# Optimization experiments

Hardware: AMD Instinct MI355X
Metric: run time of the kernel (lower is better)

Reference implementation:

```python
import jax, jax.numpy as jnp
import numpy as np

HIDDEN = 300
ATOM_FDIM = 133
BOND_ONLY_FDIM = 14
BOND_FDIM = ATOM_FDIM + BOND_ONLY_FDIM  # 147, chemprop concatenates atom feats into bond feats
DEPTH = 3
N_ATOMS = 100000
N_BONDS = 200000  # directed bonds, stored as reverse pairs (2k, 2k+1)
MAX_NB = 6
N_MOLS = 2000


def _lin(key, fan_in, fan_out):
    s = 1.0 / np.sqrt(fan_in)
    return jax.random.uniform(key, (fan_in, fan_out), jnp.float32, -s, s)


def setup_inputs() -> dict:
    key = jax.random.key(0)
    ks = jax.random.split(key, 16)
    f_atoms = jax.random.normal(ks[0], (N_ATOMS, ATOM_FDIM), jnp.float32)
    f_bonds = jax.random.normal(ks[1], (N_BONDS, BOND_FDIM), jnp.float32)
    a2b = jax.random.randint(ks[2], (N_ATOMS, MAX_NB), 0, N_BONDS, jnp.int32)
    b2a = jax.random.randint(ks[3], (N_BONDS,), 0, N_ATOMS, jnp.int32)
    b2revb = jnp.arange(N_BONDS, dtype=jnp.int32) ^ 1  # reverse-bond pairing
    graph_idx = jnp.sort(jax.random.randint(ks[4], (N_ATOMS,), 0, N_MOLS, jnp.int32))
    params = dict(
        W_i=_lin(ks[5], BOND_FDIM, HIDDEN),              # no bias in chemprop W_i
        W_h=_lin(ks[6], HIDDEN, HIDDEN),                 # no bias in chemprop W_h
        W_o=_lin(ks[7], ATOM_FDIM + HIDDEN, HIDDEN),
        b_o=jnp.zeros((HIDDEN,), jnp.float32),
        W_node=_lin(ks[8], HIDDEN, ATOM_FDIM),
        b_node=jnp.zeros((ATOM_FDIM,), jnp.float32),
        W_edge=_lin(ks[9], HIDDEN, BOND_ONLY_FDIM),
        b_edge=jnp.zeros((BOND_ONLY_FDIM,), jnp.float32),
        W_g1=_lin(ks[10], HIDDEN, HIDDEN),
        b_g1=jnp.zeros((HIDDEN,), jnp.float32),
        W_g2=_lin(ks[11], HIDDEN, 1),
        b_g2=jnp.zeros((1,), jnp.float32),
    )
    return dict(f_atoms=f_atoms, f_bonds=f_bonds, a2b=a2b, b2a=b2a,
                b2revb=b2revb, graph_idx=graph_idx, **params)


def reference(f_atoms, f_bonds, a2b, b2a, b2revb, graph_idx,
              W_i, W_h, W_o, b_o, W_node, b_node,
              W_edge, b_edge, W_g1, b_g1, W_g2, b_g2):
    # ---- chemprop bond-message MPN encoder (dropout=0) ----
    inp = f_bonds @ W_i                       # [n_bonds, H]
    msg = jax.nn.relu(inp)
    for _ in range(DEPTH - 1):
        a_msg = msg[a2b].sum(axis=1)          # gather neighbor bond msgs -> [n_atoms, H]
        msg = jax.nn.relu(inp + (a_msg[b2a] - msg[b2revb]) @ W_h)
    a_msg = msg[a2b].sum(axis=1)
    atom_hiddens = jax.nn.relu(jnp.concatenate([f_atoms, a_msg], axis=-1) @ W_o + b_o)
    # ---- graph pooling: per-molecule SUM (as in the forward loop) ----
    graph_emb = jax.ops.segment_sum(atom_hiddens, graph_idx, num_segments=N_MOLS)
    # ---- heads ----
    node_preds = atom_hiddens @ W_node + b_node
    # bond loop: visits each reverse pair once (even bond first), averages endpoint atoms
    e1 = jnp.arange(0, N_BONDS, 2)
    a1 = b2a[e1]
    a2 = b2a[b2revb[e1]]
    h_avg = 0.5 * (atom_hiddens[a1] + atom_hiddens[a2])
    edge_preds = h_avg @ W_edge + b_edge
    graph_preds = jax.nn.relu(graph_emb @ W_g1 + b_g1) @ W_g2 + b_g2
    return node_preds, edge_preds, graph_preds
```

## Files before the change

### kernel.cpp

```cpp
#include <hip/hip_runtime.h>

typedef unsigned short u16;
typedef unsigned int u32;

#define N_ATOMS 100000
#define N_BONDS 200000
#define N_EDGES 100000
#define HIDDEN 300
#define HP 320
#define ATOM_FDIM 133
#define BOND_FDIM 147
#define CATP 448
#define N_MOLS 2000

typedef __bf16 bf16x8 __attribute__((ext_vector_type(8)));
typedef float f32x4 __attribute__((ext_vector_type(4)));

__device__ __forceinline__ u16 f2bf(float f) {
    union { float f; u32 u; } x; x.f = f;
    u32 u = x.u;
    u32 r = u + 0x7fffu + ((u >> 16) & 1u);
    return (u16)(r >> 16);
}
__device__ __forceinline__ float bf2f(u16 h) {
    union { u32 u; float f; } x; x.u = ((u32)h) << 16;
    return x.f;
}

union U8 { uint4 v; u16 h[8]; };
union U4 { uint2 v; u16 h[4]; };

template<int ASRC, int EP, int KSTEPS, int NB>
__global__ __launch_bounds__(256) void k_gemmR(
    const u16* __restrict__ srcA, const float* __restrict__ fsrc,
    int M, const u16* __restrict__ Bt, int ldb, int Nout,
    const float* __restrict__ bias, const float* __restrict__ bias2,
    u16* __restrict__ O1, float* __restrict__ F1, float* __restrict__ F2,
    const u16* __restrict__ inp_in, int nwg)
{
    __shared__ __align__(16) u16 As[128 * 40];
    __shared__ __align__(16) u16 Bs[64 * 40];

    const int bid = blockIdx.x;
    const int q = nwg >> 3, r = nwg & 7;
    const int xcd = bid & 7, sidx = bid >> 3;
    const int wg = (xcd < r ? xcd * (q + 1) : r * (q + 1) + (xcd - r) * q) + sidx;

    const int n0 = (wg % NB) * 64;
    const int row0 = (wg / NB) * 128;

    const int tid = threadIdx.x;
    const int lane = tid & 63;
    const int w = tid >> 6, wr = w >> 1, wc = w & 1;
    const int lrow = lane & 15;
    const int g = lane >> 4;
    const int lkb = g * 8;

    const int rA0 = tid >> 2, kg = tid & 3, kofs = kg * 8;
    const int rA1 = rA0 + 64;
    int r0 = row0 + rA0; if (r0 >= M) r0 = M - 1;
    int r1 = row0 + rA1; if (r1 >= M) r1 = M - 1;

    auto loadA = [&](int rr, int k0) -> uint4 {
        U8 u;
        if constexpr (ASRC == 0) {
            u.v = *(const uint4*)(srcA + (size_t)rr * HP + k0 + kofs);
        } else if constexpr (ASRC == 1) {
            size_t fb = (size_t)rr * BOND_FDIM;
#pragma unroll
            for (int e = 0; e < 8; e++) {
                int col = k0 + kofs + e;
                u.h[e] = (col < BOND_FDIM) ? f2bf(fsrc[fb + col]) : (u16)0;
            }
        } else {
            int col0 = k0 + kofs;
            if (col0 < 304) {
                u.v = *(const uint4*)(srcA + (size_t)rr * HP + col0);
            } else {
                size_t fb = (size_t)rr * ATOM_FDIM;
#pragma unroll
                for (int e = 0; e < 8; e++) {
                    int col = col0 + e - 304;
                    u.h[e] = (col < ATOM_FDIM) ? f2bf(fsrc[fb + col]) : (u16)0;
                }
            }
        }
        return u.v;
    };

    const u16* pb = Bt + (size_t)(n0 + rA0) * ldb + kofs;

    uint4 va0 = loadA(r0, 0);
    uint4 va1 = loadA(r1, 0);
    uint4 vb  = *(const uint4*)pb;

    f32x4 acc[4][2] = {};

    constexpr int K = KSTEPS * 32;
    for (int k0 = 0; k0 < K; k0 += 32) {
        *(uint4*)&As[rA0 * 40 + kofs] = va0;
        *(uint4*)&As[rA1 * 40 + kofs] = va1;
        *(uint4*)&Bs[rA0 * 40 + kofs] = vb;
        __syncthreads();
        if (k0 + 32 < K) {
            va0 = loadA(r0, k0 + 32);
            va1 = loadA(r1, k0 + 32);
            vb  = *(const uint4*)(pb + k0 + 32);
        }
        bf16x8 af[4], bfr[2];
#pragma unroll
        for (int m = 0; m < 4; m++)
            af[m] = *(const bf16x8*)&As[(wr * 64 + m * 16 + lrow) * 40 + lkb];
#pragma unroll
        for (int n = 0; n < 2; n++)
            bfr[n] = *(const bf16x8*)&Bs[(wc * 32 + n * 16 + lrow) * 40 + lkb];
#pragma unroll
        for (int m = 0; m < 4; m++)
#pragma unroll
            for (int n = 0; n < 2; n++)
                acc[m][n] = __builtin_amdgcn_mfma_f32_16x16x32_bf16(bfr[n], af[m], acc[m][n], 0, 0, 0);
        __syncthreads();
    }

    if constexpr (EP == 4) {
        float* LDSf = (float*)As;
#pragma unroll
        for (int m = 0; m < 4; m++) {
            __syncthreads();
#pragma unroll
            for (int n = 0; n < 2; n++)
                *(f32x4*)&LDSf[(size_t)(wr * 16 + lrow) * 68 + wc * 32 + n * 16 + g * 4] = acc[m][n];
            __syncthreads();
#pragma unroll
            for (int i = 0; i < 8; i++) {
                const int rl = w + i * 4;
                const int grow = row0 + ((rl & 16) ? 64 : 0) + m * 16 + (rl & 15);
                const float v = LDSf[(size_t)rl * 68 + lane];
                const int col = n0 + lane;
                if (grow < M) {
                    if (col < 133) F1[(size_t)grow * 133 + col] = v + bias[col];
                    else if (col < 147) F2[(size_t)grow * 16 + (col - 133)] = v + bias2[col - 133];
                }
            }
        }
    } else {
#pragma unroll
        for (int m = 0; m < 4; m++) {
            const int row = row0 + wr * 64 + m * 16 + lrow;
            if (row >= M) continue;
#pragma unroll
            for (int n = 0; n < 2; n++) {
                const int colb = n0 + wc * 32 + n * 16 + g * 4;
                U4 o;
                if constexpr (EP == 1) {
#pragma unroll
                    for (int qq = 0; qq < 4; qq++) o.h[qq] = f2bf(acc[m][n][qq]);
                } else if constexpr (EP == 2) {
                    U4 ii; ii.v = *(const uint2*)&inp_in[(size_t)row * HP + colb];
#pragma unroll
                    for (int qq = 0; qq < 4; qq++) o.h[qq] = f2bf(acc[m][n][qq] + bf2f(ii.h[qq]));
                } else {
#pragma unroll
                    for (int qq = 0; qq < 4; qq++) {
                        float x = acc[m][n][qq] + ((colb + qq) < Nout ? bias[colb + qq] : 0.f);
                        o.h[qq] = f2bf(fmaxf(x, 0.f));
                    }
                }
                *(uint2*)&O1[(size_t)row * HP + colb] = o.v;
            }
        }
    }
}

__global__ void k_pack_wt(const float* __restrict__ W, u16* __restrict__ Bt,
                          int K, int N, int Kp, int Np)
{
    int idx = blockIdx.x * 256 + threadIdx.x;
    if (idx >= Np * Kp) return;
    int n = idx / Kp, k = idx - n * Kp;
    Bt[idx] = (n < N && k < K) ? f2bf(W[(size_t)k * N + n]) : (u16)0;
}

__global__ void k_pack_wo(const float* __restrict__ W, u16* __restrict__ Bt)
{
    int idx = blockIdx.x * 256 + threadIdx.x;
    if (idx >= 320 * CATP) return;
    int n = idx / CATP, k = idx - n * CATP;
    float v = 0.f;
    if (n < HIDDEN) {
        if (k < HIDDEN) v = W[(size_t)(ATOM_FDIM + k) * HIDDEN + n];
        else if (k >= 304 && k < 304 + ATOM_FDIM) v = W[(size_t)(k - 304) * HIDDEN + n];
    }
    Bt[idx] = f2bf(v);
}

__global__ void k_pack_wne(const float* __restrict__ Wn, const float* __restrict__ We,
                           u16* __restrict__ Bt)
{
    int idx = blockIdx.x * 256 + threadIdx.x;
    if (idx >= 320 * 320) return;
    int n = idx / 320, k = idx - n * 320;
    float v = 0.f;
    if (k < HIDDEN) {
        if (n < ATOM_FDIM) v = Wn[(size_t)k * ATOM_FDIM + n];
        else if (n < ATOM_FDIM + 14) v = We[(size_t)k * 14 + (n - ATOM_FDIM)];
    }
    Bt[idx] = f2bf(v);
}

__global__ __launch_bounds__(256) void k_aggregate(const u16* __restrict__ h,
    const int* __restrict__ a2b, u16* __restrict__ amsg)
{
    int idx = blockIdx.x * 256 + threadIdx.x;
    if (idx >= N_ATOMS * 40) return;
    int a = idx / 40, c = (idx - a * 40) * 8;
    float s[8] = {};
#pragma unroll
    for (int j = 0; j < 6; j++) {
        int b = a2b[a * 6 + j];
        U8 u; u.v = *(const uint4*)&h[(size_t)b * HP + c];
#pragma unroll
        for (int i = 0; i < 8; i++) s[i] += fmaxf(bf2f(u.h[i]), 0.f);
    }
    U8 o;
#pragma unroll
    for (int i = 0; i < 8; i++) o.h[i] = f2bf(s[i]);
    *(uint4*)&amsg[(size_t)a * HP + c] = o.v;
}

__global__ __launch_bounds__(256) void k_delta(const u16* __restrict__ amsg,
    const u16* __restrict__ h, const int* __restrict__ b2a, u16* __restrict__ dlt)
{
    int idx = blockIdx.x * 256 + threadIdx.x;
    if (idx >= N_BONDS * 40) return;
    int b = idx / 40, c = (idx - b * 40) * 8;
    int a = b2a[b];
    U8 x; x.v = *(const uint4*)&amsg[(size_t)a * HP + c];
    U8 y; y.v = *(const uint4*)&h[(size_t)(b ^ 1) * HP + c];
    U8 o;
#pragma unroll
    for (int i = 0; i < 8; i++)
        o.h[i] = f2bf(bf2f(x.h[i]) - fmaxf(bf2f(y.h[i]), 0.f));
    *(uint4*)&dlt[(size_t)b * HP + c] = o.v;
}

__global__ __launch_bounds__(256) void k_edge(const float* __restrict__ E,
    const int* __restrict__ b2a, float* __restrict__ out)
{
    int idx = blockIdx.x * 256 + threadIdx.x;
    if (idx >= N_EDGES * 7) return;
    int e = idx / 7, p = idx - e * 7;
    int a1 = b2a[2 * e], a2 = b2a[2 * e + 1];
    float2 x = *(const float2*)&E[(size_t)a1 * 16 + 2 * p];
    float2 y = *(const float2*)&E[(size_t)a2 * 16 + 2 * p];
    float2 o; o.x = 0.5f * (x.x + y.x); o.y = 0.5f * (x.y + y.y);
    *(float2*)&out[(size_t)e * 14 + 2 * p] = o;
}

__device__ __forceinline__ int lower_bound_i(const int* a, int n, int v) {
    int lo = 0, hi = n;
    while (lo < hi) { int mid = (lo + hi) >> 1; if (a[mid] < v) lo = mid + 1; else hi = mid; }
    return lo;
}
__global__ __launch_bounds__(320) void k_segsum(const u16* __restrict__ ah,
    const int* __restrict__ gidx, float* __restrict__ gemb)
{
    int g = blockIdx.x;
    int c = threadIdx.x;
    int s = lower_bound_i(gidx, N_ATOMS, g);
    int e = lower_bound_i(gidx, N_ATOMS, g + 1);
    float sum = 0.f;
    for (int a = s; a < e; a++) sum += bf2f(ah[(size_t)a * HP + c]);
    gemb[(size_t)g * HP + c] = sum;
}

__global__ __launch_bounds__(320) void k_g1(const float* __restrict__ gemb,
    const float* __restrict__ W, const float* __restrict__ b, float* __restrict__ gh)
{
    int g = blockIdx.x, j = threadIdx.x;
    float acc = 0.f;
    if (j < HIDDEN) {
        acc = b[j];
        for (int k = 0; k < HIDDEN; k++)
            acc = fmaf(gemb[(size_t)g * HP + k], W[(size_t)k * HIDDEN + j], acc);
        acc = fmaxf(acc, 0.f);
    }
    gh[(size_t)g * HP + j] = (j < HIDDEN) ? acc : 0.f;
}
__global__ __launch_bounds__(64) void k_g2(const float* __restrict__ gh,
    const float* __restrict__ W, const float* __restrict__ b, float* __restrict__ out)
{
    int g = blockIdx.x, l = threadIdx.x;
    float acc = 0.f;
    for (int j = l; j < HIDDEN; j += 64) acc += gh[(size_t)g * HP + j] * W[j];
#pragma unroll
    for (int off = 32; off; off >>= 1) acc += __shfl_down(acc, off, 64);
    if (l == 0) out[g] = acc + b[0];
}

extern "C" void kernel_launch(void* const* d_in, const int* in_sizes, int n_in,
                              void* d_out, int out_size, void* d_ws, size_t ws_size,
                              hipStream_t stream)
{
    const float* f_atoms = (const float*)d_in[0];
    const float* f_bonds = (const float*)d_in[1];
    const int* a2b    = (const int*)d_in[2];
    const int* b2a    = (const int*)d_in[3];
    const int* gidx   = (const int*)d_in[5];
    const float* W_i    = (const float*)d_in[6];
    const float* W_h    = (const float*)d_in[7];
    const float* W_o    = (const float*)d_in[8];
    const float* b_o    = (const float*)d_in[9];
    const float* W_node = (const float*)d_in[10];
    const float* b_node = (const float*)d_in[11];
    const float* W_edge = (const float*)d_in[12];
    const float* b_edge = (const float*)d_in[13];
    const float* W_g1   = (const float*)d_in[14];
    const float* b_g1   = (const float*)d_in[15];
    const float* W_g2   = (const float*)d_in[16];
    const float* b_g2   = (const float*)d_in[17];

    char* ws = (char*)d_ws;
    u16* inp   = (u16*)(ws + 0);
    u16* hA    = (u16*)(ws + 128000000);
    u16* hB    = (u16*)(ws + 256000000);
    u16* amsg  = (u16*)(ws + 384000000);
    u16* wt_i  = (u16*)(ws + 448000000);
    u16* wt_h  = (u16*)(ws + 448200000);
    u16* wt_o  = (u16*)(ws + 448500000);
    u16* wt_ne = (u16*)(ws + 448800000);
    float* gemb = (float*)(ws + 449300000);
    float* gh   = (float*)(ws + 452000000);

    float* out_node  = (float*)d_out;
    float* out_edge  = out_node + (size_t)N_ATOMS * ATOM_FDIM;
    float* out_graph = out_node + 14700000;

    dim3 blk(256);

    k_pack_wt<<<(320 * 160 + 255) / 256, blk, 0, stream>>>(W_i, wt_i, BOND_FDIM, HIDDEN, 160, 320);
    k_pack_wt<<<(320 * 320 + 255) / 256, blk, 0, stream>>>(W_h, wt_h, HIDDEN, HIDDEN, 320, 320);
    k_pack_wo<<<(320 * CATP + 255) / 256, blk, 0, stream>>>(W_o, wt_o);
    k_pack_wne<<<(320 * 320 + 255) / 256, blk, 0, stream>>>(W_node, W_edge, wt_ne);

    const int mbB = (N_BONDS + 127) / 128;
    const int mbA = (N_ATOMS + 127) / 128;
    const int gAg = (N_ATOMS * 40 + 255) / 256;
    const int gDl = (N_BONDS * 40 + 255) / 256;

    const int nwgI = 5 * mbB;
    const int nwgO = 5 * mbA;
    const int nwgH = 3 * mbA;

    k_gemmR<1, 1, 5, 5><<<nwgI, blk, 0, stream>>>(
        nullptr, f_bonds, N_BONDS, wt_i, 160, 0, nullptr, nullptr,
        inp, nullptr, nullptr, nullptr, nwgI);

    const u16* hcur = inp;
    for (int d = 0; d < 2; ++d) {
        k_aggregate<<<gAg, blk, 0, stream>>>(hcur, a2b, amsg);
        k_delta<<<gDl, blk, 0, stream>>>(amsg, hcur, b2a, hB);
        k_gemmR<0, 2, 10, 5><<<nwgI, blk, 0, stream>>>(
            hB, nullptr, N_BONDS, wt_h, 320, 0, nullptr, nullptr,
            hA, nullptr, nullptr, inp, nwgI);
        hcur = hA;
    }

    k_aggregate<<<gAg, blk, 0, stream>>>(hcur, a2b, amsg);
    u16* ah = hB;
    k_gemmR<3, 3, 14, 5><<<nwgO, blk, 0, stream>>>(
        amsg, f_atoms, N_ATOMS, wt_o, CATP, HIDDEN, b_o, nullptr,
        ah, nullptr, nullptr, nullptr, nwgO);

    float* Ebuf = (float*)inp;
    k_gemmR<0, 4, 10, 3><<<nwgH, blk, 0, stream>>>(
        ah, nullptr, N_ATOMS, wt_ne, 320, 0, b_node, b_edge,
        nullptr, out_node, Ebuf, nullptr, nwgH);

    k_edge<<<(N_EDGES * 7 + 255) / 256, blk, 0, stream>>>(Ebuf, b2a, out_edge);

    k_segsum<<<N_MOLS, 320, 0, stream>>>(ah, gidx, gemb);
    k_g1<<<N_MOLS, 320, 0, stream>>>(gemb, W_g1, b_g1, gh);
    k_g2<<<N_MOLS, 64, 0, stream>>>(gh, W_g2, b_g2, out_graph);
}
```

Baseline: 1.143 ms.

## Use direct global-to-LDS loads in GEMMs and pre-pack fp32 inputs to bf16

Replaces the register-staged GEMM A/B tile loads with global_load_lds direct-to-LDS copies and drops the fp32-to-bf16 conversion from inside the GEMM loaders. f_bonds and f_atoms are now converted by separate pack kernels, and the aggregate output is written straight into a concatenated buffer. The residual input is prefetched before the K loop, and launch bounds now request 4 waves/SIMD occupancy. The cost is extra pack passes and the loss of register double-buffering: each k-step now issues its load and waits on a barrier without overlap, and the unpadded LDS stride may cause bank conflicts.

```diff
diff --git a/kernel.cpp b/kernel.cpp
--- a/kernel.cpp
+++ b/kernel.cpp
@@ -30,16 +30,21 @@
 union U8 { uint4 v; u16 h[8]; };
 union U4 { uint2 v; u16 h[4]; };
 
-template<int ASRC, int EP, int KSTEPS, int NB>
-__global__ __launch_bounds__(256) void k_gemmR(
-    const u16* __restrict__ srcA, const float* __restrict__ fsrc,
-    int M, const u16* __restrict__ Bt, int ldb, int Nout,
+#define GL16(gp, lp) __builtin_amdgcn_global_load_lds( \
+    (const __attribute__((address_space(1))) u32*)(gp), \
+    (__attribute__((address_space(3))) u32*)(lp), 16, 0, 0)
+
+template<int EP, int KSTEPS, int LDA, int NB>
+__global__ __launch_bounds__(256, 4) void k_gemmG(
+    const u16* __restrict__ A, int M,
+    const u16* __restrict__ Bt, int ldb, int Nout,
     const float* __restrict__ bias, const float* __restrict__ bias2,
     u16* __restrict__ O1, float* __restrict__ F1, float* __restrict__ F2,
     const u16* __restrict__ inp_in, int nwg)
 {
-    __shared__ __align__(16) u16 As[128 * 40];
-    __shared__ __align__(16) u16 Bs[64 * 40];
+    __shared__ __align__(16) u16 SM[128 * 32 + 64 * 32];
+    u16* As = SM;
+    u16* Bs = SM + 128 * 32;
 
     const int bid = blockIdx.x;
     const int q = nwg >> 3, r = nwg & 7;
@@ -51,69 +56,53 @@
 
     const int tid = threadIdx.x;
     const int lane = tid & 63;
-    const int w = tid >> 6, wr = w >> 1, wc = w & 1;
+    const int wv = tid >> 6;
+    const int wr = wv >> 1, wc = wv & 1;
     const int lrow = lane & 15;
     const int g = lane >> 4;
-    const int lkb = g * 8;
-
-    const int rA0 = tid >> 2, kg = tid & 3, kofs = kg * 8;
-    const int rA1 = rA0 + 64;
-    int r0 = row0 + rA0; if (r0 >= M) r0 = M - 1;
-    int r1 = row0 + rA1; if (r1 >= M) r1 = M - 1;
-
-    auto loadA = [&](int rr, int k0) -> uint4 {
-        U8 u;
-        if constexpr (ASRC == 0) {
-            u.v = *(const uint4*)(srcA + (size_t)rr * HP + k0 + kofs);
-        } else if constexpr (ASRC == 1) {
-            size_t fb = (size_t)rr * BOND_FDIM;
-#pragma unroll
-            for (int e = 0; e < 8; e++) {
-                int col = k0 + kofs + e;
-                u.h[e] = (col < BOND_FDIM) ? f2bf(fsrc[fb + col]) : (u16)0;
-            }
-        } else {
-            int col0 = k0 + kofs;
-            if (col0 < 304) {
-                u.v = *(const uint4*)(srcA + (size_t)rr * HP + col0);
-            } else {
-                size_t fb = (size_t)rr * ATOM_FDIM;
-#pragma unroll
-                for (int e = 0; e < 8; e++) {
-                    int col = col0 + e - 304;
-                    u.h[e] = (col < ATOM_FDIM) ? f2bf(fsrc[fb + col]) : (u16)0;
-                }
+
+    const int lr = lane >> 2, lc = lane & 3;
+    int arow0 = row0 + wv * 32 + lr;
+    int arow1 = arow0 + 16;
+    if (arow0 >= M) arow0 = M - 1;
+    if (arow1 >= M) arow1 = M - 1;
+    const u16* gA0 = A + (size_t)arow0 * LDA + lc * 8;
+    const u16* gA1 = A + (size_t)arow1 * LDA + lc * 8;
+    const u16* gB  = Bt + (size_t)(n0 + wv * 16 + lr) * ldb + lc * 8;
+    u16* lA0 = &As[(wv * 32) * 32];
+    u16* lA1 = &As[(wv * 32 + 16) * 32];
+    u16* lB  = &Bs[(wv * 16) * 32];
+
+    U4 ii[8];
+    if constexpr (EP == 2) {
+#pragma unroll
+        for (int m = 0; m < 4; m++) {
+            const int row = row0 + wr * 64 + m * 16 + lrow;
+#pragma unroll
+            for (int n = 0; n < 2; n++) {
+                if (row < M)
+                    ii[m * 2 + n].v = *(const uint2*)&inp_in[
+                        (size_t)row * HP + n0 + wc * 32 + n * 16 + g * 4];
             }
         }
-        return u.v;
-    };
-
-    const u16* pb = Bt + (size_t)(n0 + rA0) * ldb + kofs;
-
-    uint4 va0 = loadA(r0, 0);
-    uint4 va1 = loadA(r1, 0);
-    uint4 vb  = *(const uint4*)pb;
+    }
 
     f32x4 acc[4][2] = {};
 
-    constexpr int K = KSTEPS * 32;
-    for (int k0 = 0; k0 < K; k0 += 32) {
-        *(uint4*)&As[rA0 * 40 + kofs] = va0;
-        *(uint4*)&As[rA1 * 40 + kofs] = va1;
-        *(uint4*)&Bs[rA0 * 40 + kofs] = vb;
+#pragma unroll
+    for (int ks = 0; ks < KSTEPS; ks++) {
+        const int k0 = ks * 32;
+        GL16(gA0 + k0, lA0);
+        GL16(gA1 + k0, lA1);
+        GL16(gB + k0, lB);
         __syncthreads();
-        if (k0 + 32 < K) {
-            va0 = loadA(r0, k0 + 32);
-            va1 = loadA(r1, k0 + 32);
-            vb  = *(const uint4*)(pb + k0 + 32);
-        }
         bf16x8 af[4], bfr[2];
 #pragma unroll
         for (int m = 0; m < 4; m++)
-            af[m] = *(const bf16x8*)&As[(wr * 64 + m * 16 + lrow) * 40 + lkb];
+            af[m] = *(const bf16x8*)&As[(wr * 64 + m * 16 + lrow) * 32 + g * 8];
 #pragma unroll
         for (int n = 0; n < 2; n++)
-            bfr[n] = *(const bf16x8*)&Bs[(wc * 32 + n * 16 + lrow) * 40 + lkb];
+            bfr[n] = *(const bf16x8*)&Bs[(wc * 32 + n * 16 + lrow) * 32 + g * 8];
 #pragma unroll
         for (int m = 0; m < 4; m++)
 #pragma unroll
@@ -123,7 +112,7 @@
     }
 
     if constexpr (EP == 4) {
-        float* LDSf = (float*)As;
+        float* LDSf = (float*)SM;
 #pragma unroll
         for (int m = 0; m < 4; m++) {
             __syncthreads();
@@ -133,7 +122,7 @@
             __syncthreads();
 #pragma unroll
             for (int i = 0; i < 8; i++) {
-                const int rl = w + i * 4;
+                const int rl = wv + i * 4;
                 const int grow = row0 + ((rl & 16) ? 64 : 0) + m * 16 + (rl & 15);
                 const float v = LDSf[(size_t)rl * 68 + lane];
                 const int col = n0 + lane;
@@ -156,9 +145,8 @@
 #pragma unroll
                     for (int qq = 0; qq < 4; qq++) o.h[qq] = f2bf(acc[m][n][qq]);
                 } else if constexpr (EP == 2) {
-                    U4 ii; ii.v = *(const uint2*)&inp_in[(size_t)row * HP + colb];
-#pragma unroll
-                    for (int qq = 0; qq < 4; qq++) o.h[qq] = f2bf(acc[m][n][qq] + bf2f(ii.h[qq]));
+#pragma unroll
+                    for (int qq = 0; qq < 4; qq++) o.h[qq] = f2bf(acc[m][n][qq] + bf2f(ii[m * 2 + n].h[qq]));
                 } else {
 #pragma unroll
                     for (int qq = 0; qq < 4; qq++) {
@@ -208,6 +196,35 @@
     Bt[idx] = f2bf(v);
 }
 
+__global__ __launch_bounds__(256) void k_pack_bonds(const float* __restrict__ fb, u16* __restrict__ out)
+{
+    int idx = blockIdx.x * 256 + threadIdx.x;
+    if (idx >= N_BONDS * 20) return;
+    int b = idx / 20, c0 = (idx - b * 20) * 8;
+    U8 u;
+#pragma unroll
+    for (int e = 0; e < 8; e++) {
+        int col = c0 + e;
+        u.h[e] = (col < BOND_FDIM) ? f2bf(fb[(size_t)b * BOND_FDIM + col]) : (u16)0;
+    }
+    *(uint4*)&out[(size_t)b * 160 + c0] = u.v;
+}
+
+__global__ __launch_bounds__(256) void k_cat_fa(const float* __restrict__ fa, u16* __restrict__ cat)
+{
+    int idx = blockIdx.x * 256 + threadIdx.x;
+    if (idx >= N_ATOMS * 18) return;
+    int a = idx / 18, c0 = 304 + (idx - a * 18) * 8;
+    U8 u;
+#pragma unroll
+    for (int e = 0; e < 8; e++) {
+        int fc = c0 + e - 304;
+        u.h[e] = (fc < ATOM_FDIM) ? f2bf(fa[(size_t)a * ATOM_FDIM + fc]) : (u16)0;
+    }
+    *(uint4*)&cat[(size_t)a * CATP + c0] = u.v;
+}
+
+template<int OST>
 __global__ __launch_bounds__(256) void k_aggregate(const u16* __restrict__ h,
     const int* __restrict__ a2b, u16* __restrict__ amsg)
 {
@@ -225,7 +242,7 @@
     U8 o;
 #pragma unroll
     for (int i = 0; i < 8; i++) o.h[i] = f2bf(s[i]);
-    *(uint4*)&amsg[(size_t)a * HP + c] = o.v;
+    *(uint4*)&amsg[(size_t)a * OST + c] = o.v;
 }
 
 __global__ __launch_bounds__(256) void k_delta(const u16* __restrict__ amsg,
@@ -347,35 +364,40 @@
     const int mbA = (N_ATOMS + 127) / 128;
     const int gAg = (N_ATOMS * 40 + 255) / 256;
     const int gDl = (N_BONDS * 40 + 255) / 256;
-
     const int nwgI = 5 * mbB;
     const int nwgO = 5 * mbA;
     const int nwgH = 3 * mbA;
 
-    k_gemmR<1, 1, 5, 5><<<nwgI, blk, 0, stream>>>(
-        nullptr, f_bonds, N_BONDS, wt_i, 160, 0, nullptr, nullptr,
+    u16* fb16 = hA;
+    k_pack_bonds<<<(N_BONDS * 20 + 255) / 256, blk, 0, stream>>>(f_bonds, fb16);
+
+    k_gemmG<1, 5, 160, 5><<<nwgI, blk, 0, stream>>>(
+        fb16, N_BONDS, wt_i, 160, 0, nullptr, nullptr,
         inp, nullptr, nullptr, nullptr, nwgI);
 
     const u16* hcur = inp;
     for (int d = 0; d < 2; ++d) {
-        k_aggregate<<<gAg, blk, 0, stream>>>(hcur, a2b, amsg);
+        k_aggregate<HP><<<gAg, blk, 0, stream>>>(hcur, a2b, amsg);
         k_delta<<<gDl, blk, 0, stream>>>(amsg, hcur, b2a, hB);
-        k_gemmR<0, 2, 10, 5><<<nwgI, blk, 0, stream>>>(
-            hB, nullptr, N_BONDS, wt_h, 320, 0, nullptr, nullptr,
+        k_gemmG<2, 10, 320, 5><<<nwgI, blk, 0, stream>>>(
+            hB, N_BONDS, wt_h, 320, 0, nullptr, nullptr,
             hA, nullptr, nullptr, inp, nwgI);
         hcur = hA;
     }
 
-    k_aggregate<<<gAg, blk, 0, stream>>>(hcur, a2b, amsg);
+    u16* catbuf = inp;
+    k_aggregate<CATP><<<gAg, blk, 0, stream>>>(hcur, a2b, catbuf);
+    k_cat_fa<<<(N_ATOMS * 18 + 255) / 256, blk, 0, stream>>>(f_atoms, catbuf);
+
     u16* ah = hB;
-    k_gemmR<3, 3, 14, 5><<<nwgO, blk, 0, stream>>>(
-        amsg, f_atoms, N_ATOMS, wt_o, CATP, HIDDEN, b_o, nullptr,
+    k_gemmG<3, 14, 448, 5><<<nwgO, blk, 0, stream>>>(
+        catbuf, N_ATOMS, wt_o, CATP, HIDDEN, b_o, nullptr,
         ah, nullptr, nullptr, nullptr, nwgO);
 
-    float* Ebuf = (float*)inp;
-    k_gemmR<0, 4, 10, 3><<<nwgH, blk, 0, stream>>>(
-        ah, nullptr, N_ATOMS, wt_ne, 320, 0, b_node, b_edge,
-        nullptr, out_node, Ebuf, nullptr, nwgH);
+    float* Ebuf = (float*)amsg;
+    k_gemmG<4, 10, 320, 3><<<nwgH, blk, 0, stream>>>(
+        ah, N_ATOMS, wt_ne, 320, 0, b_node, b_edge,
+        nullptr, out_node, Ebuf, nwgH ? nullptr : nullptr, nwgH);
 
     k_edge<<<(N_EDGES * 7 + 255) / 256, blk, 0, stream>>>(Ebuf, b2a, out_edge);
 
```

Measured after the change: 1.006 ms. 12.0% less time.
